# Kernel optimization log

Measured on AMD Instinct MI355X. Metric: run time of the kernel, lower is better.

The kernel has to match this reference:

```python
import math
import jax, jax.numpy as jnp
import numpy as np

N_KINDS = 8
D_MODEL = 256
B_FEAT = 24  # Fourier bands; MLP input dim is 2*B_FEAT
SIGMA = 8.0


def setup_inputs() -> dict:
    key = jax.random.key(0)
    ks = jax.random.split(key, 8)
    N, S = 32, 2048
    values = jax.random.normal(ks[0], (N, S, 1), dtype=jnp.float32)
    kinds = jax.random.randint(ks[1], (N, S), 0, N_KINDS, dtype=jnp.int32)
    # Frozen Fourier projection matrix (torch: randn(in_dim, B) * sigma, requires_grad=False)
    Bmat = jax.random.normal(ks[2], (1, B_FEAT), dtype=jnp.float32) * SIGMA
    # Kind embedding table
    kind_emb = jax.random.normal(ks[3], (N_KINDS, D_MODEL), dtype=jnp.float32) * 0.02
    # Per-kind two-layer MLP params
    W1 = jax.random.normal(ks[4], (N_KINDS, 2 * B_FEAT, D_MODEL), dtype=jnp.float32) / math.sqrt(2 * B_FEAT)
    b1 = jnp.zeros((N_KINDS, D_MODEL), dtype=jnp.float32)
    W2 = jax.random.normal(ks[5], (N_KINDS, D_MODEL, D_MODEL), dtype=jnp.float32) / math.sqrt(D_MODEL)
    b2 = jnp.zeros((N_KINDS, D_MODEL), dtype=jnp.float32)
    return {"values": values, "kinds": kinds, "Bmat": Bmat,
            "kind_emb": kind_emb, "W1": W1, "b1": b1, "W2": W2, "b2": b2}


def reference(values, kinds, Bmat, kind_emb, W1, b1, W2, b2):
    N, S, _ = values.shape
    T = N * S
    d = kind_emb.shape[-1]
    # Fourier features: [T, 2B]
    y = (2.0 * math.pi) * values.reshape(T, 1) @ Bmat  # [T, B]
    ff = jnp.concatenate([jnp.sin(y), jnp.cos(y)], axis=-1)  # [T, 2B]
    kinds_flat = kinds.reshape(T)
    out = jnp.zeros((T, d), dtype=values.dtype)
    # kinds partition the tokens, so masked combine == the torch scatter-assign
    for k in range(kind_emb.shape[0]):
        h = jax.nn.gelu(ff @ W1[k] + b1[k], approximate=False)  # torch GELU is exact erf
        o = h @ W2[k] + b2[k]  # [T, d]
        out = jnp.where((kinds_flat == k)[:, None], o, out)
    return out.reshape(N, S, d) + kind_emb[kinds]
```

## Files before the change

### kernel.cpp

```cpp
#include <hip/hip_runtime.h>
#include <hip/hip_bf16.h>
#include <math.h>


#define NK 8
#define DM 256
#define TMAX 65536
#define NBLK 256
#define W1PK 16384
#define W2PK 65536
#define LDSTRIDE 262

typedef __attribute__((ext_vector_type(8))) short   s16x8;
typedef __attribute__((ext_vector_type(8))) __bf16  bf16x8;
typedef __attribute__((ext_vector_type(4))) float   f32x4;
typedef __attribute__((ext_vector_type(2))) float   f32x2;

__device__ __align__(16) int g_counts[NK * 32];
__device__ int   g_bucket[(size_t)NK * TMAX];
__device__ __align__(16) short g_W1p[(size_t)NK * W1PK];
__device__ __align__(16) short g_W2p[(size_t)NK * W2PK];

static __device__ __forceinline__ short f2bf(float f) {
    __hip_bfloat16 h = __float2bfloat16(f);
    return __builtin_bit_cast(short, h);
}

static __device__ __forceinline__ short pkbf(float f) {
    unsigned u = __builtin_bit_cast(unsigned, f);
    return (short)((u + 0x8000u) >> 16);
}

static __device__ __forceinline__ f32x4 mfma16(s16x8 a, s16x8 b, f32x4 c) {
    return __builtin_amdgcn_mfma_f32_16x16x32_bf16(
        __builtin_bit_cast(bf16x8, a), __builtin_bit_cast(bf16x8, b), c, 0, 0, 0);
}

static __device__ __forceinline__ float gelu_fast(float x) {
    float t1 = x * x;
    float m  = fmaf(0.0713548162726f, t1, 1.59576912161f);
    float z  = m * x;
    float e  = __expf(-z);
    return x * __frcp_rn(1.0f + e);
}

__global__ __launch_bounds__(256) void prep_kernel(const float* __restrict__ W1,
                                                   const float* __restrict__ W2,
                                                   const int* __restrict__ kinds, int T) {
    const int tid = threadIdx.x;
    const int bid = blockIdx.x;
    if (bid < 80) {
        __shared__ float ld[32 * LDSTRIDE];
        const int isW1 = (bid >= 64);
        int kind, kt;
        if (isW1) { kind = (bid - 64) >> 1; kt = (bid - 64) & 1; }
        else      { kind = bid >> 3;        kt = bid & 7; }
        #pragma unroll
        for (int i = 0; i < 8; ++i) {
            int f = tid + i * 256;
            int row = f >> 6, col = (f & 63) * 4;
            int kk = kt * 32 + row;
            f32x4 v = (f32x4){0.f, 0.f, 0.f, 0.f};
            if (isW1) {
                if (kk < 48) v = *(const f32x4*)(W1 + ((size_t)kind * 48 + kk) * DM + col);
            } else {
                v = *(const f32x4*)(W2 + ((size_t)kind * DM + kk) * DM + col);
            }
            float* dst = &ld[row * LDSTRIDE + col];
            *(f32x2*)dst       = (f32x2){v[0], v[1]};
            *(f32x2*)(dst + 2) = (f32x2){v[2], v[3]};
        }
        __syncthreads();
        short* outp = isW1 ? (g_W1p + (size_t)kind * W1PK) : (g_W2p + (size_t)kind * W2PK);
        #pragma unroll
        for (int i = 0; i < 4; ++i) {
            int g = tid + i * 256;
            int ntile = g >> 6, l = g & 63;
            int kk0 = (l >> 4) * 8, n = ntile * 16 + (l & 15);
            s16x8 v;
            #pragma unroll
            for (int j = 0; j < 8; ++j) v[j] = f2bf(ld[(kk0 + j) * LDSTRIDE + n]);
            *(s16x8*)(outp + ((size_t)(kt * 16 + ntile) * 64 + l) * 8) = v;
        }
    } else {
        __shared__ int wcnt[4][NK];
        __shared__ int base_s[NK];
        const int b = bid - 80;
        const int wave = tid >> 6, lane = tid & 63;
        int t = b * 256 + tid;
        int k = (t < T) ? kinds[t] : -1;
        int rank = 0;
        #pragma unroll
        for (int kk = 0; kk < NK; ++kk) {
            unsigned long long m = __ballot(k == kk);
            if (lane == 0) wcnt[wave][kk] = __popcll(m);
            if (k == kk) rank = __popcll(m & ((1ull << lane) - 1ull));
        }
        __syncthreads();
        if (tid < NK) {
            int ws = 0;
            #pragma unroll
            for (int w = 0; w < 4; ++w) { int c = wcnt[w][tid]; wcnt[w][tid] = ws; ws += c; }
            base_s[tid] = atomicAdd(&g_counts[tid * 32], ws);
        }
        __syncthreads();
        if (k >= 0)
            g_bucket[(size_t)k * T + base_s[k] + wcnt[wave][k] + rank] = t;
    }
}

__global__ __launch_bounds__(512, 4) void fproj_gemm(
    const float* __restrict__ values, const float* __restrict__ Bmat,
    const float* __restrict__ kind_emb, const float* __restrict__ b1,
    const float* __restrict__ b2, float* __restrict__ out, int T)
{
    int cnts[NK];
    #pragma unroll
    for (int i = 0; i < NK; ++i) cnts[i] = g_counts[i * 32];
    const int bid = blockIdx.x;
    int k = -1, m0 = 0, cum = 0, cnt = 0;
    #pragma unroll
    for (int kk = 0; kk < NK; ++kk) {
        int tk = (cnts[kk] + 63) >> 6;
        if (k < 0 && bid < cum + tk) { k = kk; m0 = (bid - cum) * 64; cnt = cnts[kk]; }
        cum += tk;
    }
    if (k < 0) return;
    const int valid = min(64, cnt - m0);
    const int* buck = g_bucket + (size_t)k * T + m0;

    __shared__ short Hpack[16384];

    const int tid  = threadIdx.x;
    const int wv   = tid >> 6;
    const int lane = tid & 63;
    const int quad = lane >> 4;
    const int cl   = lane & 15;

    float vm[4];
    #pragma unroll
    for (int mt = 0; mt < 4; ++mt) {
        int row = mt * 16 + cl;
        vm[mt] = (row < valid) ? values[buck[row]] : 0.0f;
    }
    float bb0[8], bb1[8];
    const float add0 = (quad == 3) ? 0.25f : 0.0f;
    #pragma unroll
    for (int j = 0; j < 8; ++j) {
        int b0 = (quad == 3) ? j : quad * 8 + j;
        bb0[j] = Bmat[b0];
        int b1i = min(8 * (quad + 1) + j, 23);
        bb1[j] = Bmat[b1i];
    }
    s16x8 a0[4], a1[4];
    #pragma unroll
    for (int mt = 0; mt < 4; ++mt) {
        float v = vm[mt];
        #pragma unroll
        for (int j = 0; j < 8; ++j) {
            float r0 = __builtin_amdgcn_fractf(fmaf(v, bb0[j], add0));
            a0[mt][j] = pkbf(__builtin_amdgcn_sinf(r0));
            float r1 = __builtin_amdgcn_fractf(fmaf(v, bb1[j], 0.25f));
            float c1 = __builtin_amdgcn_sinf(r1);
            a1[mt][j] = pkbf((quad < 2) ? c1 : 0.0f);
        }
    }

    f32x4 acc[4][2];
    #pragma unroll
    for (int mt = 0; mt < 4; ++mt)
        #pragma unroll
        for (int nt = 0; nt < 2; ++nt) acc[mt][nt] = (f32x4){0.f, 0.f, 0.f, 0.f};
    const s16x8* B1p = (const s16x8*)(g_W1p + (size_t)k * W1PK);
    #pragma unroll
    for (int kt = 0; kt < 2; ++kt) {
        s16x8 bf[2];
        #pragma unroll
        for (int nt = 0; nt < 2; ++nt) bf[nt] = B1p[(kt * 16 + wv * 2 + nt) * 64 + lane];
        #pragma unroll
        for (int mt = 0; mt < 4; ++mt) {
            s16x8 a = kt ? a1[mt] : a0[mt];
            #pragma unroll
            for (int nt = 0; nt < 2; ++nt) acc[mt][nt] = mfma16(a, bf[nt], acc[mt][nt]);
        }
    }

    #pragma unroll
    for (int nt = 0; nt < 2; ++nt) {
        int c = wv * 32 + nt * 16 + cl;
        float bias = b1[k * DM + c];
        int kt2 = c >> 5, q2 = (c >> 3) & 3, j2 = c & 7;
        #pragma unroll
        for (int mt = 0; mt < 4; ++mt) {
            short* hp = Hpack + (kt2 * 4 + mt) * 512 + q2 * 128 + j2;
            #pragma unroll
            for (int r = 0; r < 4; ++r) {
                int m = quad * 4 + r;
                float h = gelu_fast(acc[mt][nt][r] + bias);
                hp[m * 8] = pkbf(h);
            }
        }
    }
    __syncthreads();

    float addc[2];
    #pragma unroll
    for (int nt = 0; nt < 2; ++nt) {
        int c = wv * 32 + nt * 16 + cl;
        addc[nt] = b2[k * DM + c] + kind_emb[k * DM + c];
    }

    f32x4 acc2[4][2];
    #pragma unroll
    for (int mt = 0; mt < 4; ++mt)
        #pragma unroll
        for (int nt = 0; nt < 2; ++nt) acc2[mt][nt] = (f32x4){0.f, 0.f, 0.f, 0.f};
    const s16x8* Hp  = (const s16x8*)Hpack;
    const s16x8* B2p = (const s16x8*)(g_W2p + (size_t)k * W2PK);
    #pragma unroll
    for (int kt = 0; kt < 8; ++kt) {
        s16x8 am[4];
        #pragma unroll
        for (int mt = 0; mt < 4; ++mt) am[mt] = Hp[(kt * 4 + mt) * 64 + lane];
        s16x8 bf[2];
        #pragma unroll
        for (int nt = 0; nt < 2; ++nt) bf[nt] = B2p[(kt * 16 + wv * 2 + nt) * 64 + lane];
        #pragma unroll
        for (int mt = 0; mt < 4; ++mt)
            #pragma unroll
            for (int nt = 0; nt < 2; ++nt) acc2[mt][nt] = mfma16(am[mt], bf[nt], acc2[mt][nt]);
    }

    #pragma unroll
    for (int mt = 0; mt < 4; ++mt)
        #pragma unroll
        for (int r = 0; r < 4; ++r) {
            int row = mt * 16 + quad * 4 + r;
            if (row < valid) {
                size_t ro = (size_t)buck[row] * DM;
                #pragma unroll
                for (int nt = 0; nt < 2; ++nt) {
                    int c = wv * 32 + nt * 16 + cl;
                    __builtin_nontemporal_store(acc2[mt][nt][r] + addc[nt], out + ro + c);
                }
            }
        }
}

extern "C" void kernel_launch(void* const* d_in, const int* in_sizes, int n_in,
                              void* d_out, int out_size, void* d_ws, size_t ws_size,
                              hipStream_t stream) {
    const float* values   = (const float*)d_in[0];
    const int*   kinds    = (const int*)  d_in[1];
    const float* Bmat     = (const float*)d_in[2];
    const float* kind_emb = (const float*)d_in[3];
    const float* W1       = (const float*)d_in[4];
    const float* b1       = (const float*)d_in[5];
    const float* W2       = (const float*)d_in[6];
    const float* b2       = (const float*)d_in[7];
    float* out = (float*)d_out;
    const int T = in_sizes[0];

    static void* cnt_addr = nullptr;
    if (!cnt_addr) (void)hipGetSymbolAddress(&cnt_addr, HIP_SYMBOL(g_counts));
    hipMemsetAsync(cnt_addr, 0, sizeof(int) * NK * 32, stream);

    prep_kernel<<<dim3(80 + NBLK), dim3(256), 0, stream>>>(W1, W2, kinds, T);
    fproj_gemm<<<dim3(T / 64 + NK), dim3(512), 0, stream>>>(values, Bmat, kind_emb,
                                                            b1, b2, out, T);
}
```

Baseline: 120.9 us.

## Replace counts memset with last-block ticket reset and hoist weight loads

Removes the per-call hipMemsetAsync of the bucket counters. The second kernel now resets them through a last-block-done atomic ticket, which drops one stream operation from each launch. It also hoists the W1 fragment loads, the bias and the kind-embedding loads ahead of the Fourier feature computation so their memory latency overlaps with the sin work. The ticket scheme assumes the counters start at zero on the first call (true for device globals) and that no run aborts midway.

```diff
diff --git a/kernel.cpp b/kernel.cpp
--- a/kernel.cpp
+++ b/kernel.cpp
@@ -17,6 +17,7 @@
 typedef __attribute__((ext_vector_type(2))) float   f32x2;
 
 __device__ __align__(16) int g_counts[NK * 32];
+__device__ int   g_done;
 __device__ int   g_bucket[(size_t)NK * TMAX];
 __device__ __align__(16) short g_W1p[(size_t)NK * W1PK];
 __device__ __align__(16) short g_W2p[(size_t)NK * W2PK];
@@ -109,6 +110,17 @@
     }
 }
 
+static __device__ __forceinline__ void finish_ticket(int nblocks) {
+    __threadfence();
+    int old = atomicAdd(&g_done, 1);
+    if (old == nblocks - 1) {
+        g_done = 0;
+        #pragma unroll
+        for (int i = 0; i < NK; ++i) g_counts[i * 32] = 0;
+        __threadfence();
+    }
+}
+
 __global__ __launch_bounds__(512, 4) void fproj_gemm(
     const float* __restrict__ values, const float* __restrict__ Bmat,
     const float* __restrict__ kind_emb, const float* __restrict__ b1,
@@ -118,6 +130,7 @@
     #pragma unroll
     for (int i = 0; i < NK; ++i) cnts[i] = g_counts[i * 32];
     const int bid = blockIdx.x;
+    const int tid = threadIdx.x;
     int k = -1, m0 = 0, cum = 0, cnt = 0;
     #pragma unroll
     for (int kk = 0; kk < NK; ++kk) {
@@ -125,17 +138,33 @@
         if (k < 0 && bid < cum + tk) { k = kk; m0 = (bid - cum) * 64; cnt = cnts[kk]; }
         cum += tk;
     }
-    if (k < 0) return;
+    if (k < 0) {
+        if (tid == 0) finish_ticket((int)gridDim.x);
+        return;
+    }
     const int valid = min(64, cnt - m0);
     const int* buck = g_bucket + (size_t)k * T + m0;
 
     __shared__ short Hpack[16384];
 
-    const int tid  = threadIdx.x;
     const int wv   = tid >> 6;
     const int lane = tid & 63;
     const int quad = lane >> 4;
     const int cl   = lane & 15;
+
+    const s16x8* B1p = (const s16x8*)(g_W1p + (size_t)k * W1PK);
+    s16x8 bfp[2][2];
+    #pragma unroll
+    for (int kt = 0; kt < 2; ++kt)
+        #pragma unroll
+        for (int nt = 0; nt < 2; ++nt) bfp[kt][nt] = B1p[(kt * 16 + wv * 2 + nt) * 64 + lane];
+    float bias1[2], addc[2];
+    #pragma unroll
+    for (int nt = 0; nt < 2; ++nt) {
+        int c = wv * 32 + nt * 16 + cl;
+        bias1[nt] = b1[k * DM + c];
+        addc[nt]  = b2[k * DM + c] + kind_emb[k * DM + c];
+    }
 
     float vm[4];
     #pragma unroll
@@ -171,24 +200,19 @@
     for (int mt = 0; mt < 4; ++mt)
         #pragma unroll
         for (int nt = 0; nt < 2; ++nt) acc[mt][nt] = (f32x4){0.f, 0.f, 0.f, 0.f};
-    const s16x8* B1p = (const s16x8*)(g_W1p + (size_t)k * W1PK);
     #pragma unroll
     for (int kt = 0; kt < 2; ++kt) {
-        s16x8 bf[2];
-        #pragma unroll
-        for (int nt = 0; nt < 2; ++nt) bf[nt] = B1p[(kt * 16 + wv * 2 + nt) * 64 + lane];
         #pragma unroll
         for (int mt = 0; mt < 4; ++mt) {
             s16x8 a = kt ? a1[mt] : a0[mt];
             #pragma unroll
-            for (int nt = 0; nt < 2; ++nt) acc[mt][nt] = mfma16(a, bf[nt], acc[mt][nt]);
+            for (int nt = 0; nt < 2; ++nt) acc[mt][nt] = mfma16(a, bfp[kt][nt], acc[mt][nt]);
         }
     }
 
     #pragma unroll
     for (int nt = 0; nt < 2; ++nt) {
         int c = wv * 32 + nt * 16 + cl;
-        float bias = b1[k * DM + c];
         int kt2 = c >> 5, q2 = (c >> 3) & 3, j2 = c & 7;
         #pragma unroll
         for (int mt = 0; mt < 4; ++mt) {
@@ -196,19 +220,12 @@
             #pragma unroll
             for (int r = 0; r < 4; ++r) {
                 int m = quad * 4 + r;
-                float h = gelu_fast(acc[mt][nt][r] + bias);
+                float h = gelu_fast(acc[mt][nt][r] + bias1[nt]);
                 hp[m * 8] = pkbf(h);
             }
         }
     }
     __syncthreads();
-
-    float addc[2];
-    #pragma unroll
-    for (int nt = 0; nt < 2; ++nt) {
-        int c = wv * 32 + nt * 16 + cl;
-        addc[nt] = b2[k * DM + c] + kind_emb[k * DM + c];
-    }
 
     f32x4 acc2[4][2];
     #pragma unroll
@@ -245,6 +262,8 @@
                 }
             }
         }
+
+    if (tid == 0) finish_ticket((int)gridDim.x);
 }
 
 extern "C" void kernel_launch(void* const* d_in, const int* in_sizes, int n_in,
@@ -261,10 +280,6 @@
     float* out = (float*)d_out;
     const int T = in_sizes[0];
 
-    static void* cnt_addr = nullptr;
-    if (!cnt_addr) (void)hipGetSymbolAddress(&cnt_addr, HIP_SYMBOL(g_counts));
-    hipMemsetAsync(cnt_addr, 0, sizeof(int) * NK * 32, stream);
-
     prep_kernel<<<dim3(80 + NBLK), dim3(256), 0, stream>>>(W1, W2, kinds, T);
     fproj_gemm<<<dim3(T / 64 + NK), dim3(512), 0, stream>>>(values, Bmat, kind_emb,
                                                             b1, b2, out, T);
```

Measured after the change: 155.4 us. 1.28x slower.
